# Kernel tuning notes

Hardware: AMD Instinct MI355X
Metric: run time of the kernel (lower is better)

## Reference

```python
import jax, jax.numpy as jnp
import numpy as np

B, T, D = 8, 1024, 16
QUANTILE = 0.5
EPS_T = 1e-6


def setup_inputs() -> dict:
    key = jax.random.key(0)
    k1, k2 = jax.random.split(key)
    z = jax.random.normal(k1, (B, T, D), dtype=jnp.float32)
    variances = jax.random.uniform(k2, (B, T, D), dtype=jnp.float32)
    length_scales = jnp.ones((D,), dtype=jnp.float32)  # nn.Parameter init
    sigmas = jnp.ones((D,), dtype=jnp.float32)         # nn.Parameter init
    return {"z": z, "variances": variances,
            "length_scales": length_scales, "sigmas": sigmas}


def reference(z, variances, length_scales, sigmas):
    b, t, d = z.shape
    dt = z.dtype
    N = b * t
    zf = z.reshape(N, d)          # [N, D] flattened per-dim samples
    vf = variances.reshape(N, d)  # [N, D]

    # quantile-threshold mask per latent dim (linear-interp quantile, as torch)
    thr = jnp.quantile(vf, QUANTILE, axis=0)          # [D]
    m = (vf <= thr).astype(dt)                        # [N, D] 0/1 mask

    # time index for every flattened point: arange(T) tiled over batch
    tt = jnp.tile(jnp.arange(t, dtype=dt), b)         # [N]
    # pairwise weight W_ij = 1 / (|t_i - t_j| + eps); shared across dims
    W = 1.0 / (jnp.abs(tt[:, None] - tt[None, :]) + EPS_T)  # [N, N]

    # masked pairwise mean of (z_i - z_j)^2 * W_ij, algebraically:
    #   sum_ij m_i m_j (z_i - z_j)^2 W_ij = 2 (u^T W m - v^T W v)
    # with u = m*z^2, v = m*z (diagonal contributes 0 since m^2 = m).
    V = m * zf                                        # [N, D]
    U = V * zf                                        # [N, D]
    WM = W @ jnp.concatenate([m, V], axis=1)          # [N, 2D] single GEMM
    Wm, WV = WM[:, :d], WM[:, d:]
    S = 2.0 * (jnp.sum(U * Wm, axis=0) - jnp.sum(V * WV, axis=0))  # [D]

    n = jnp.sum(m, axis=0)                            # [D] selected counts
    mean_ratio = S / (n * n)                          # mean over N_sel^2 pairs
    ls_est = jax.lax.stop_gradient(jnp.sqrt(mean_ratio))  # .detach() in torch

    # (unbiased variance estimate; only used for 'cauchy' kernel, kept for parity)
    mu = jnp.sum(V, axis=0) / n
    var_est = jax.lax.stop_gradient(
        jnp.sum(m * (zf - mu[None, :]) ** 2, axis=0) / (n - 1.0))

    enough = n >= 2.0
    length_scale = jnp.where(enough, ls_est, jnp.exp(length_scales))  # [D]
    _sigma = jnp.where(enough, var_est, jnp.exp(sigmas))  # unused for rbf

    # rbf kernel per dim: exp(-(ti - tj)^2 / ls^2), [D, T, T]
    ts = jnp.arange(t, dtype=dt)
    dist2 = (ts[None, :] - ts[:, None]) ** 2          # [T, T]
    K = jnp.exp(-dist2[None, :, :] / (length_scale[:, None, None] ** 2))
    # repeat over batch -> [B, D, T, T] (covariance of the MVN prior; loc is 0)
    return jnp.broadcast_to(K[None], (b, d, t, t))
```

## Files before the change

### kernel.cpp

```cpp
#include <hip/hip_runtime.h>

typedef float vfloat4 __attribute__((ext_vector_type(4)));

#define TT 1024
#define BB 8
#define DD 16
#define NN 8192

__device__ inline float untr(unsigned u) {
    unsigned b = (u & 0x80000000u) ? (u & 0x7fffffffu) : ~u;
    return __uint_as_float(b);
}

__global__ __launch_bounds__(1024) void median_k(const float* __restrict__ v,
                                                 float* __restrict__ thr) {
    __shared__ unsigned key[NN];
    __shared__ unsigned hist[2048];
    __shared__ unsigned wsum[16];
    __shared__ unsigned found_bin, found_cum;
    __shared__ unsigned s_cle, s_min;
    const int d = blockIdx.x;
    const int tid = threadIdx.x;
    const int wid = tid >> 6, lane = tid & 63;

    for (int i = tid; i < NN; i += 1024) {
        unsigned b = __float_as_uint(v[i * DD + d]);
        key[i] = (b & 0x80000000u) ? ~b : (b | 0x80000000u);
    }
    if (tid == 0) { s_cle = 0; s_min = 0xFFFFFFFFu; }
    __syncthreads();

    unsigned prefix = 0;
    unsigned r = 4095;
    int matched_bits = 0;
    int shift = 32;
    const int chunk_bits[3] = {11, 11, 10};
#pragma unroll
    for (int pass = 0; pass < 3; ++pass) {
        const int bits = chunk_bits[pass];
        shift -= bits;
        const int nb = 1 << bits;
        hist[tid] = 0; hist[tid + 1024] = 0;
        __syncthreads();
        for (int i = tid; i < NN; i += 1024) {
            unsigned k = key[i];
            if (matched_bits == 0 || (k >> (shift + bits)) == prefix)
                atomicAdd(&hist[(k >> shift) & (unsigned)(nb - 1)], 1u);
        }
        __syncthreads();
        unsigned h0 = 0, h1 = 0, s2 = 0;
        if (tid < nb / 2) { h0 = hist[2 * tid]; h1 = hist[2 * tid + 1]; s2 = h0 + h1; }
        unsigned inc = s2;
        for (int o = 1; o < 64; o <<= 1) {
            unsigned t = __shfl_up(inc, o);
            if (lane >= o) inc += t;
        }
        if (lane == 63) wsum[wid] = inc;
        __syncthreads();
        if (tid < 16) {
            unsigned x = wsum[tid], ix = x;
            for (int o = 1; o < 16; o <<= 1) {
                unsigned t = __shfl_up(ix, o);
                if (lane >= o) ix += t;
            }
            wsum[tid] = ix - x;
        }
        __syncthreads();
        if (tid < nb / 2) {
            unsigned cum = wsum[wid] + (inc - s2);
            if (r >= cum && r < cum + h0)            { found_bin = 2u * tid;     found_cum = cum; }
            else if (r >= cum + h0 && r < cum + s2)  { found_bin = 2u * tid + 1; found_cum = cum + h0; }
        }
        __syncthreads();
        prefix = (prefix << bits) | found_bin;
        r -= found_cum;
        matched_bits += bits;
    }
    const unsigned A = prefix;

    unsigned cle = 0, mg = 0xFFFFFFFFu;
    for (int i = tid; i < NN; i += 1024) {
        unsigned k = key[i];
        if (k <= A) cle++;
        else mg = min(mg, k);
    }
    for (int o = 32; o; o >>= 1) {
        cle += __shfl_xor(cle, o);
        mg = min(mg, (unsigned)__shfl_xor(mg, o));
    }
    if (lane == 0) { atomicAdd(&s_cle, cle); atomicMin(&s_min, mg); }
    __syncthreads();
    if (tid == 0) {
        unsigned Bk = (s_cle >= 4097u) ? A : s_min;
        thr[d] = 0.5f * (untr(A) + untr(Bk));
    }
}

__global__ __launch_bounds__(256) void colsum_k(const float* __restrict__ z,
                                                const float* __restrict__ v,
                                                const float* __restrict__ thr,
                                                float* __restrict__ ms,
                                                float* __restrict__ vs,
                                                float* __restrict__ us,
                                                float* __restrict__ Sacc,
                                                float* __restrict__ nacc) {
    const int g = blockIdx.x * 256 + threadIdx.x;
    if (blockIdx.x == 0) {
        if (threadIdx.x < DD)            Sacc[threadIdx.x] = 0.f;
        else if (threadIdx.x < 2 * DD)   nacc[threadIdx.x - DD] = 0.f;
    }
    const int d = g & (DD - 1);
    const float t = thr[d];
    float sm = 0.f, sv = 0.f, su = 0.f;
#pragma unroll
    for (int b = 0; b < BB; ++b) {
        float vv = v[b * (TT * DD) + g];
        float zz = z[b * (TT * DD) + g];
        if (vv <= t) { sm += 1.f; sv += zz; su += zz * zz; }
    }
    ms[g] = sm; vs[g] = sv; us[g] = su;
}

__global__ __launch_bounds__(64) void scale_k(const float* __restrict__ ms,
                                              const float* __restrict__ vs,
                                              const float* __restrict__ us,
                                              float* __restrict__ Sacc,
                                              float* __restrict__ nacc) {
    __shared__ float sm[TT], sv[TT], wt[TT];
    const int d = blockIdx.x >> 4;
    const int chunk = blockIdx.x & 15;
    const int tid = threadIdx.x;
    for (int q = tid; q < TT; q += 64) {
        sm[q] = ms[q * DD + d];
        sv[q] = vs[q * DD + d];
        wt[q] = 1.0f / ((float)q + 1e-6f);
    }
    __syncthreads();
    const int p = chunk * 64 + tid;
    const float a = us[p * DD + d];
    const float c = sv[p];
    float acc = 0.f;
#pragma unroll 4
    for (int q = 0; q < TT; ++q) {
        int ad = p - q; ad = ad < 0 ? -ad : ad;
        acc = fmaf(wt[ad], fmaf(a, sm[q], -(c * sv[q])), acc);
    }
    float npart = sm[p];
    for (int o = 32; o; o >>= 1) {
        acc += __shfl_xor(acc, o);
        npart += __shfl_xor(npart, o);
    }
    if (tid == 0) {
        atomicAdd(&Sacc[d], 2.0f * acc);
        atomicAdd(&nacc[d], npart);
    }
}

__global__ __launch_bounds__(64) void ls_k(const float* __restrict__ Sacc,
                                           const float* __restrict__ nacc,
                                           const float* __restrict__ lsin,
                                           float* __restrict__ inv_out) {
    const int d = threadIdx.x;
    if (d < DD) {
        const float n = nacc[d], S = Sacc[d];
        float invv;
        if (n >= 2.0f) invv = (n * n) / S;
        else { const float e = expf(lsin[d]); invv = 1.0f / (e * e); }
        inv_out[d] = invv;
    }
}

__global__ __launch_bounds__(256) void write_k(const float* __restrict__ inv_ls2,
                                               float* __restrict__ out) {
    const int bid = blockIdx.x;
    const int d = bid >> 10;
    const int i = bid & (TT - 1);
    const float inv = inv_ls2[d];
    const int j0 = threadIdx.x * 4;
    vfloat4 val;
#pragma unroll
    for (int jj = 0; jj < 4; ++jj) {
        const int diff = (j0 + jj) - i;
        const float f = (float)(diff * diff);
        val[jj] = __expf(-f * inv);
    }
    const size_t base = ((size_t)d << 20) | ((size_t)i << 10) | (size_t)j0;
#pragma unroll
    for (int b = 0; b < BB; ++b) {
        vfloat4* p = (vfloat4*)(out + ((size_t)b << 24) + base);
        __builtin_nontemporal_store(val, p);
    }
}

extern "C" void kernel_launch(void* const* d_in, const int* in_sizes, int n_in,
                              void* d_out, int out_size, void* d_ws, size_t ws_size,
                              hipStream_t stream) {
    const float* z    = (const float*)d_in[0];
    const float* v    = (const float*)d_in[1];
    const float* lsin = (const float*)d_in[2];
    float* out = (float*)d_out;

    float* ws   = (float*)d_ws;
    float* thr  = ws;
    float* inv  = ws + 16;
    float* Sacc = ws + 32;
    float* nacc = ws + 48;
    float* ms   = ws + 64;
    float* vs   = ms + TT * DD;
    float* us   = vs + TT * DD;

    median_k<<<DD, 1024, 0, stream>>>(v, thr);
    colsum_k<<<(TT * DD) / 256, 256, 0, stream>>>(z, v, thr, ms, vs, us, Sacc, nacc);
    scale_k<<<DD * 16, 64, 0, stream>>>(ms, vs, us, Sacc, nacc);
    ls_k<<<1, 64, 0, stream>>>(Sacc, nacc, lsin, inv);
    write_k<<<DD * TT, 256, 0, stream>>>(inv, out);
}
```

Before: 574.5 us.

## Fuse column sums into pairwise kernel and fold length-scale into write kernel

Removes the separate colsum and ls kernels. Each pairwise-stats block now recomputes the masked per-time sums directly from z and v, and the write kernel computes the inverse squared length scale inline. Accumulator zeroing moves into the median kernel. This cuts two kernel launches and the intermediate global buffers, at the cost of redundant recomputation (16 blocks per dim each reload all 8x1024 strided values) and a per-block divide in the write kernel.

Result: slower. 632.3 us (+10.1%).

```diff
diff --git a/kernel.cpp b/kernel.cpp
--- a/kernel.cpp
+++ b/kernel.cpp
@@ -13,7 +13,9 @@
 }
 
 __global__ __launch_bounds__(1024) void median_k(const float* __restrict__ v,
-                                                 float* __restrict__ thr) {
+                                                 float* __restrict__ thr,
+                                                 float* __restrict__ Sacc,
+                                                 float* __restrict__ nacc) {
     __shared__ unsigned key[NN];
     __shared__ unsigned hist[2048];
     __shared__ unsigned wsum[16];
@@ -22,6 +24,8 @@
     const int d = blockIdx.x;
     const int tid = threadIdx.x;
     const int wid = tid >> 6, lane = tid & 63;
+
+    if (tid == 0) { Sacc[d] = 0.f; nacc[d] = 0.f; }
 
     for (int i = tid; i < NN; i += 1024) {
         unsigned b = __float_as_uint(v[i * DD + d]);
@@ -96,48 +100,34 @@
     }
 }
 
-__global__ __launch_bounds__(256) void colsum_k(const float* __restrict__ z,
-                                                const float* __restrict__ v,
-                                                const float* __restrict__ thr,
-                                                float* __restrict__ ms,
-                                                float* __restrict__ vs,
-                                                float* __restrict__ us,
-                                                float* __restrict__ Sacc,
-                                                float* __restrict__ nacc) {
-    const int g = blockIdx.x * 256 + threadIdx.x;
-    if (blockIdx.x == 0) {
-        if (threadIdx.x < DD)            Sacc[threadIdx.x] = 0.f;
-        else if (threadIdx.x < 2 * DD)   nacc[threadIdx.x - DD] = 0.f;
-    }
-    const int d = g & (DD - 1);
-    const float t = thr[d];
-    float sm = 0.f, sv = 0.f, su = 0.f;
-#pragma unroll
-    for (int b = 0; b < BB; ++b) {
-        float vv = v[b * (TT * DD) + g];
-        float zz = z[b * (TT * DD) + g];
-        if (vv <= t) { sm += 1.f; sv += zz; su += zz * zz; }
-    }
-    ms[g] = sm; vs[g] = sv; us[g] = su;
-}
-
-__global__ __launch_bounds__(64) void scale_k(const float* __restrict__ ms,
-                                              const float* __restrict__ vs,
-                                              const float* __restrict__ us,
+__global__ __launch_bounds__(64) void stats_k(const float* __restrict__ z,
+                                              const float* __restrict__ v,
+                                              const float* __restrict__ thr,
                                               float* __restrict__ Sacc,
                                               float* __restrict__ nacc) {
     __shared__ float sm[TT], sv[TT], wt[TT];
     const int d = blockIdx.x >> 4;
     const int chunk = blockIdx.x & 15;
     const int tid = threadIdx.x;
+    const int p = chunk * 64 + tid;
+    const float t = thr[d];
+
+    float su = 0.f;
     for (int q = tid; q < TT; q += 64) {
-        sm[q] = ms[q * DD + d];
-        sv[q] = vs[q * DD + d];
+        float s_m = 0.f, s_v = 0.f, s_u = 0.f;
+#pragma unroll
+        for (int b = 0; b < BB; ++b) {
+            const float vv = v[b * (TT * DD) + q * DD + d];
+            const float zz = z[b * (TT * DD) + q * DD + d];
+            if (vv <= t) { s_m += 1.f; s_v += zz; s_u += zz * zz; }
+        }
+        sm[q] = s_m; sv[q] = s_v;
         wt[q] = 1.0f / ((float)q + 1e-6f);
+        if (q == p) su = s_u;
     }
     __syncthreads();
-    const int p = chunk * 64 + tid;
-    const float a = us[p * DD + d];
+
+    const float a = su;
     const float c = sv[p];
     float acc = 0.f;
 #pragma unroll 4
@@ -156,26 +146,19 @@
     }
 }
 
-__global__ __launch_bounds__(64) void ls_k(const float* __restrict__ Sacc,
-                                           const float* __restrict__ nacc,
-                                           const float* __restrict__ lsin,
-                                           float* __restrict__ inv_out) {
-    const int d = threadIdx.x;
-    if (d < DD) {
-        const float n = nacc[d], S = Sacc[d];
-        float invv;
-        if (n >= 2.0f) invv = (n * n) / S;
-        else { const float e = expf(lsin[d]); invv = 1.0f / (e * e); }
-        inv_out[d] = invv;
-    }
-}
-
-__global__ __launch_bounds__(256) void write_k(const float* __restrict__ inv_ls2,
+__global__ __launch_bounds__(256) void write_k(const float* __restrict__ Sacc,
+                                               const float* __restrict__ nacc,
+                                               const float* __restrict__ lsin,
                                                float* __restrict__ out) {
     const int bid = blockIdx.x;
     const int d = bid >> 10;
     const int i = bid & (TT - 1);
-    const float inv = inv_ls2[d];
+
+    const float n = nacc[d], S = Sacc[d];
+    float inv;
+    if (n >= 2.0f) inv = (n * n) / S;
+    else { const float e = __expf(lsin[d]); inv = 1.0f / (e * e); }
+
     const int j0 = threadIdx.x * 4;
     vfloat4 val;
 #pragma unroll
@@ -202,16 +185,10 @@
 
     float* ws   = (float*)d_ws;
     float* thr  = ws;
-    float* inv  = ws + 16;
-    float* Sacc = ws + 32;
-    float* nacc = ws + 48;
-    float* ms   = ws + 64;
-    float* vs   = ms + TT * DD;
-    float* us   = vs + TT * DD;
+    float* Sacc = ws + 16;
+    float* nacc = ws + 32;
 
-    median_k<<<DD, 1024, 0, stream>>>(v, thr);
-    colsum_k<<<(TT * DD) / 256, 256, 0, stream>>>(z, v, thr, ms, vs, us, Sacc, nacc);
-    scale_k<<<DD * 16, 64, 0, stream>>>(ms, vs, us, Sacc, nacc);
-    ls_k<<<1, 64, 0, stream>>>(Sacc, nacc, lsin, inv);
-    write_k<<<DD * TT, 256, 0, stream>>>(inv, out);
+    median_k<<<DD, 1024, 0, stream>>>(v, thr, Sacc, nacc);
+    stats_k<<<DD * 16, 64, 0, stream>>>(z, v, thr, Sacc, nacc);
+    write_k<<<DD * TT, 256, 0, stream>>>(Sacc, nacc, lsin, out);
 }
```
